# Performance work log

Hardware: AMD Instinct MI355X
Metric: run time of the kernel (lower is better)

## Reference

```python
import jax, jax.numpy as jnp
import numpy as np

W = 50          # Sakoe-Chiba window half-width (|i-j| <= W)
BIG = 1e9       # finite 'infinity' so gradients stay NaN-free
EPS = 1e-8      # matches torch.cosine_similarity eps


def setup_inputs() -> dict:
    key = jax.random.key(0)
    k1, k2 = jax.random.split(key)
    x1 = jax.random.normal(k1, (64, 512, 256), dtype=jnp.float32)
    x2 = jax.random.normal(k2, (64, 512, 256), dtype=jnp.float32)
    return {"x1": x1, "x2": x2}


def _cosine_cost(x1, x2):
    # cost[b,i,j] = 1 - cos_sim(x1[b,i], x2[b,j])
    num = jnp.einsum('bid,bjd->bij', x1, x2)
    n1 = jnp.maximum(jnp.sqrt(jnp.sum(x1 * x1, axis=-1)), EPS)  # [B,T1]
    n2 = jnp.maximum(jnp.sqrt(jnp.sum(x2 * x2, axis=-1)), EPS)  # [B,T2]
    return 1.0 - num / (n1[:, :, None] * n2[:, None, :])


def _dtw_acc(cost, w):
    # Anti-diagonal wavefront DP: acc[i,j] = cost[i,j] + min(acc[i-1,j], acc[i,j-1], acc[i-1,j-1])
    # with the Sakoe-Chiba band |i-j| <= w. Returns acc[T1-1, T2-1] per batch.
    B, T1, T2 = cost.shape
    ii = jnp.arange(T1)
    dt = cost.dtype

    def step(carry, d):
        prev1, prev2 = carry                       # diagonals d-1 and d-2, each [B,T1] indexed by i
        jj = d - ii                                # column index for each row i on diagonal d
        valid = (jj >= 0) & (jj < T2) & (jnp.abs(ii - jj) <= w)
        # gather cost[b, i, d-i]
        cdiag = jnp.take_along_axis(
            cost, jnp.clip(jj, 0, T2 - 1)[None, :, None], axis=2)[..., 0]  # [B,T1]
        pad = jnp.full((B, 1), BIG, dt)
        p1_im1 = jnp.concatenate([pad, prev1[:, :-1]], axis=1)  # acc[i-1, j]   (diag d-1, i-1)
        p2_im1 = jnp.concatenate([pad, prev2[:, :-1]], axis=1)  # acc[i-1, j-1] (diag d-2, i-1)
        m = jnp.minimum(jnp.minimum(prev1, p1_im1), p2_im1)     # prev1 = acc[i, j-1]
        m = jnp.where((ii == 0) & (jj == 0), jnp.zeros((), dt), m)  # DP origin
        new = jnp.where(valid, cdiag + m, jnp.full((), BIG, dt))
        return (new, prev1), None

    init = (jnp.full((B, T1), BIG, dt), jnp.full((B, T1), BIG, dt))
    (last, _), _ = jax.lax.scan(step, init, jnp.arange(T1 + T2 - 1))
    return last[:, T1 - 1]  # acc[-1, -1]


def reference(x1, x2):
    cost = _cosine_cost(x1, x2)       # [B,T1,T2]
    scores = _dtw_acc(cost, W)        # [B]
    return scores[:, None]            # [B,1], matches unsqueeze(-1)
```

## Files before the change

kernel.cpp:

```cpp
#include <hip/hip_runtime.h>

#define BIGF 1e9f
#define TT 512
#define DD 256
#define NB 64
#define DROWS 1088
#define SAK 40
#define CST 66

typedef float floatx16 __attribute__((ext_vector_type(16)));
typedef __bf16 bf16x8 __attribute__((ext_vector_type(8)));

__device__ __forceinline__ float dpp_wave_shr1(float x, float oldv) {
  int r = __builtin_amdgcn_update_dpp(__builtin_bit_cast(int, oldv),
                                      __builtin_bit_cast(int, x),
                                      0x138, 0xF, 0xF, false);
  return __builtin_bit_cast(float, r);
}
__device__ __forceinline__ float dpp_wave_shl1(float x, float oldv) {
  int r = __builtin_amdgcn_update_dpp(__builtin_bit_cast(int, oldv),
                                      __builtin_bit_cast(int, x),
                                      0x130, 0xF, 0xF, false);
  return __builtin_bit_cast(float, r);
}

__global__ __launch_bounds__(256) void cost_kernel(const float* __restrict__ x1,
                                                   const float* __restrict__ x2,
                                                   float* __restrict__ diag) {
  const int n = blockIdx.x;
  const int b = n & 63;
  const int m = n >> 6;
  const int it = m & 7;
  const int jt = m >> 3;
  const int i0 = it * 64;
  const int j0 = i0 - 50 + jt * 64;

  __shared__ __align__(16) float sC[64 * CST];
  __bf16* sA = (__bf16*)sC;
  __bf16* sB = ((__bf16*)sC) + 64 * SAK;
  __shared__ float rA[64];
  __shared__ float rB[64];

  const int t = threadIdx.x;
  const int lane = t & 63;
  const int w = t >> 6;
  const int wi = w >> 1;
  const int wj = w & 1;
  const int ln = lane & 31;
  const int kh = lane >> 5;

  float* db = diag + (size_t)b * (DROWS * 64);

  if (m == 0) {
    for (int r = w; r < 180; r += 4) {
      const int d = (r < 64) ? r : r + 908;
      const int p = d & 1;
      const int i = (d >> 1) + lane + p - 25;
      const int j = d - i;
      const int k = 2 * lane + p;
      if (k > 100 || (unsigned)i >= TT || (unsigned)j >= TT)
        db[(size_t)d * 64 + lane] = BIGF;
    }
  }

  const int sr = t >> 2;
  const int sq = t & 3;
  const float* x1b = x1 + (size_t)b * (TT * DD);
  const float* x2b = x2 + (size_t)b * (TT * DD);
  int gj = j0 + sr;
  gj = gj < 0 ? 0 : (gj > TT - 1 ? TT - 1 : gj);
  const float* pAg = x1b + (size_t)(i0 + sr) * DD + sq * 8;
  const float* pBg = x2b + (size_t)gj * DD + sq * 8;
  __bf16* dA = sA + sr * SAK + sq * 8;
  __bf16* dB = sB + sr * SAK + sq * 8;

  const __bf16* fAp = sA + (wi * 32 + ln) * SAK + kh * 8;
  const __bf16* fBp = sB + (wj * 32 + ln) * SAK + kh * 8;

  floatx16 acc = {};
  float pa = 0.f, pb = 0.f;

  for (int kc = 0; kc < DD; kc += 32) {
    const float4 a0 = *(const float4*)(pAg + kc);
    const float4 a1 = *(const float4*)(pAg + kc + 4);
    const float4 b0 = *(const float4*)(pBg + kc);
    const float4 b1 = *(const float4*)(pBg + kc + 4);
    pa += a0.x * a0.x + a0.y * a0.y + a0.z * a0.z + a0.w * a0.w;
    pa += a1.x * a1.x + a1.y * a1.y + a1.z * a1.z + a1.w * a1.w;
    pb += b0.x * b0.x + b0.y * b0.y + b0.z * b0.z + b0.w * b0.w;
    pb += b1.x * b1.x + b1.y * b1.y + b1.z * b1.z + b1.w * b1.w;
    __syncthreads();
    {
      bf16x8 va, vb;
      va[0] = (__bf16)a0.x; va[1] = (__bf16)a0.y; va[2] = (__bf16)a0.z; va[3] = (__bf16)a0.w;
      va[4] = (__bf16)a1.x; va[5] = (__bf16)a1.y; va[6] = (__bf16)a1.z; va[7] = (__bf16)a1.w;
      vb[0] = (__bf16)b0.x; vb[1] = (__bf16)b0.y; vb[2] = (__bf16)b0.z; vb[3] = (__bf16)b0.w;
      vb[4] = (__bf16)b1.x; vb[5] = (__bf16)b1.y; vb[6] = (__bf16)b1.z; vb[7] = (__bf16)b1.w;
      *(bf16x8*)dA = va;
      *(bf16x8*)dB = vb;
    }
    __syncthreads();
    const bf16x8 fa0 = *(const bf16x8*)fAp;
    const bf16x8 fb0 = *(const bf16x8*)fBp;
    const bf16x8 fa1 = *(const bf16x8*)(fAp + 16);
    const bf16x8 fb1 = *(const bf16x8*)(fBp + 16);
    acc = __builtin_amdgcn_mfma_f32_32x32x16_bf16(fa0, fb0, acc, 0, 0, 0);
    acc = __builtin_amdgcn_mfma_f32_32x32x16_bf16(fa1, fb1, acc, 0, 0, 0);
  }

  pa += __shfl_xor(pa, 1, 64); pa += __shfl_xor(pa, 2, 64);
  pb += __shfl_xor(pb, 1, 64); pb += __shfl_xor(pb, 2, 64);
  if (sq == 0) {
    rA[sr] = 1.0f / fmaxf(sqrtf(pa), 1e-8f);
    rB[sr] = 1.0f / fmaxf(sqrtf(pb), 1e-8f);
  }
  __syncthreads();

  {
    const int rj = wj * 32 + ln;
    const float r2 = rB[rj];
#pragma unroll
    for (int reg = 0; reg < 16; ++reg) {
      const int ri = wi * 32 + (reg & 3) + 8 * (reg >> 2) + 4 * kh;
      sC[ri * CST + rj] = 1.0f - acc[reg] * rA[ri] * r2;
    }
  }
  __syncthreads();

  {
    const int d0 = i0 + j0;
    const int a65 = 65 * lane;
#pragma unroll 4
    for (int rr = 0; rr < 32; ++rr) {
      const int r = 4 * rr + w;
      const int d = d0 + r;
      const int p = d & 1;
      const int roff = ((d + p - 50) >> 1) - i0;
      const int ri = lane + roff;
      const int rj = r - ri;
      const int kband = 2 * lane + p;
      const int jg = j0 + rj;
      if (((unsigned)ri < 64u) & ((unsigned)rj < 64u) & (kband <= 100) &
          ((unsigned)jg < (unsigned)TT)) {
        db[(size_t)d * 64 + lane] = sC[a65 + 65 * roff + r];
      }
    }
  }
}

__global__ __launch_bounds__(64) void dtw_dp_kernel(const float* __restrict__ diag,
                                                    float* __restrict__ out) {
  const int b = blockIdx.x;
  const int l = threadIdx.x;
  const bool inv_odd = (l >= 50);
  const bool inv_even = (l >= 51);
  const float* base = diag + (size_t)b * (DROWS * 64);
  const float* pO = base + 64 + l;
  const float* pE = base + 128 + l;
  float cr[32];
#pragma unroll
  for (int t = 0; t < 16; ++t) {
    cr[2 * t] = *pO; pO += 128;
    cr[2 * t + 1] = *pE; pE += 128;
  }
  float prev2 = BIGF;
  const float c00 = base[25];
  float prev1 = (l == 25) ? c00 : BIGF;
  float ans = BIGF;
  for (int it = 0; it < 32; ++it) {
#pragma unroll
    for (int u = 0; u < 16; ++u) {
      const float c1 = inv_odd ? BIGF : cr[2 * u];
      cr[2 * u] = *pO; pO += 128;
      const float sh = dpp_wave_shl1(prev1, BIGF);
      const float m3 = fminf(fminf(prev1, sh), prev2);
      prev2 = prev1;
      prev1 = c1 + m3;
      const float c2 = inv_even ? BIGF : cr[2 * u + 1];
      cr[2 * u + 1] = *pE; pE += 128;
      const float sh2 = dpp_wave_shr1(prev1, BIGF);
      const float m32 = fminf(fminf(sh2, prev1), prev2);
      prev2 = prev1;
      prev1 = c2 + m32;
      if (u == 14 && it == 31) ans = prev1;
    }
  }
  if (l == 25) out[b] = ans;
}

extern "C" void kernel_launch(void* const* d_in, const int* in_sizes, int n_in,
                              void* d_out, int out_size, void* d_ws, size_t ws_size,
                              hipStream_t stream) {
  const float* x1 = (const float*)d_in[0];
  const float* x2 = (const float*)d_in[1];
  float* out = (float*)d_out;
  float* diag = (float*)d_ws;

  cost_kernel<<<NB * 24, 256, 0, stream>>>(x1, x2, diag);
  dtw_dp_kernel<<<NB, 64, 0, stream>>>(diag, out);
}
```

Baseline: 127.1 us.

## Process two cost tiles per block and deepen DP cost prefetch

The cost kernel now launches 768 blocks, each handling two 64x64 tiles in a loop. Tiles are remapped so consecutive blocks cover 8 different batches. This cuts the launch to roughly 3 blocks per CU and changes how loads spread across memory. The DP kernel doubles its register prefetch buffer from 32 to 64 cost values to hide more global load latency, at the cost of more registers and a deeper prologue.

```diff
diff --git a/kernel.cpp b/kernel.cpp
--- a/kernel.cpp
+++ b/kernel.cpp
@@ -27,13 +27,9 @@
 __global__ __launch_bounds__(256) void cost_kernel(const float* __restrict__ x1,
                                                    const float* __restrict__ x2,
                                                    float* __restrict__ diag) {
-  const int n = blockIdx.x;
-  const int b = n & 63;
-  const int m = n >> 6;
-  const int it = m & 7;
-  const int jt = m >> 3;
-  const int i0 = it * 64;
-  const int j0 = i0 - 50 + jt * 64;
+  const int p = blockIdx.x;
+  const int x = p & 7;
+  const int pl = p >> 3;
 
   __shared__ __align__(16) float sC[64 * CST];
   __bf16* sA = (__bf16*)sC;
@@ -49,100 +45,111 @@
   const int ln = lane & 31;
   const int kh = lane >> 5;
 
-  float* db = diag + (size_t)b * (DROWS * 64);
-
-  if (m == 0) {
-    for (int r = w; r < 180; r += 4) {
-      const int d = (r < 64) ? r : r + 908;
-      const int p = d & 1;
-      const int i = (d >> 1) + lane + p - 25;
-      const int j = d - i;
-      const int k = 2 * lane + p;
-      if (k > 100 || (unsigned)i >= TT || (unsigned)j >= TT)
-        db[(size_t)d * 64 + lane] = BIGF;
-    }
-  }
-
   const int sr = t >> 2;
   const int sq = t & 3;
-  const float* x1b = x1 + (size_t)b * (TT * DD);
-  const float* x2b = x2 + (size_t)b * (TT * DD);
-  int gj = j0 + sr;
-  gj = gj < 0 ? 0 : (gj > TT - 1 ? TT - 1 : gj);
-  const float* pAg = x1b + (size_t)(i0 + sr) * DD + sq * 8;
-  const float* pBg = x2b + (size_t)gj * DD + sq * 8;
   __bf16* dA = sA + sr * SAK + sq * 8;
   __bf16* dB = sB + sr * SAK + sq * 8;
-
   const __bf16* fAp = sA + (wi * 32 + ln) * SAK + kh * 8;
   const __bf16* fBp = sB + (wj * 32 + ln) * SAK + kh * 8;
 
-  floatx16 acc = {};
-  float pa = 0.f, pb = 0.f;
-
-  for (int kc = 0; kc < DD; kc += 32) {
-    const float4 a0 = *(const float4*)(pAg + kc);
-    const float4 a1 = *(const float4*)(pAg + kc + 4);
-    const float4 b0 = *(const float4*)(pBg + kc);
-    const float4 b1 = *(const float4*)(pBg + kc + 4);
-    pa += a0.x * a0.x + a0.y * a0.y + a0.z * a0.z + a0.w * a0.w;
-    pa += a1.x * a1.x + a1.y * a1.y + a1.z * a1.z + a1.w * a1.w;
-    pb += b0.x * b0.x + b0.y * b0.y + b0.z * b0.z + b0.w * b0.w;
-    pb += b1.x * b1.x + b1.y * b1.y + b1.z * b1.z + b1.w * b1.w;
+  for (int kt = 0; kt < 2; ++kt) {
+    const int T = pl + 96 * kt;
+    const int bhi = T / 24;
+    const int m = T - bhi * 24;
+    const int b = bhi * 8 + x;
+    const int it = m & 7;
+    const int jt = m >> 3;
+    const int i0 = it * 64;
+    const int j0 = i0 - 50 + jt * 64;
+
+    float* db = diag + (size_t)b * (DROWS * 64);
+
+    if (m == 0) {
+      for (int r = w; r < 180; r += 4) {
+        const int d = (r < 64) ? r : r + 908;
+        const int pp = d & 1;
+        const int i = (d >> 1) + lane + pp - 25;
+        const int j = d - i;
+        const int k = 2 * lane + pp;
+        if (k > 100 || (unsigned)i >= TT || (unsigned)j >= TT)
+          db[(size_t)d * 64 + lane] = BIGF;
+      }
+    }
+
+    const float* x1b = x1 + (size_t)b * (TT * DD);
+    const float* x2b = x2 + (size_t)b * (TT * DD);
+    int gj = j0 + sr;
+    gj = gj < 0 ? 0 : (gj > TT - 1 ? TT - 1 : gj);
+    const float* pAg = x1b + (size_t)(i0 + sr) * DD + sq * 8;
+    const float* pBg = x2b + (size_t)gj * DD + sq * 8;
+
+    floatx16 acc = {};
+    float pa = 0.f, pb = 0.f;
+
+    for (int kc = 0; kc < DD; kc += 32) {
+      const float4 a0 = *(const float4*)(pAg + kc);
+      const float4 a1 = *(const float4*)(pAg + kc + 4);
+      const float4 b0 = *(const float4*)(pBg + kc);
+      const float4 b1 = *(const float4*)(pBg + kc + 4);
+      pa += a0.x * a0.x + a0.y * a0.y + a0.z * a0.z + a0.w * a0.w;
+      pa += a1.x * a1.x + a1.y * a1.y + a1.z * a1.z + a1.w * a1.w;
+      pb += b0.x * b0.x + b0.y * b0.y + b0.z * b0.z + b0.w * b0.w;
+      pb += b1.x * b1.x + b1.y * b1.y + b1.z * b1.z + b1.w * b1.w;
+      __syncthreads();
+      {
+        bf16x8 va, vb;
+        va[0] = (__bf16)a0.x; va[1] = (__bf16)a0.y; va[2] = (__bf16)a0.z; va[3] = (__bf16)a0.w;
+        va[4] = (__bf16)a1.x; va[5] = (__bf16)a1.y; va[6] = (__bf16)a1.z; va[7] = (__bf16)a1.w;
+        vb[0] = (__bf16)b0.x; vb[1] = (__bf16)b0.y; vb[2] = (__bf16)b0.z; vb[3] = (__bf16)b0.w;
+        vb[4] = (__bf16)b1.x; vb[5] = (__bf16)b1.y; vb[6] = (__bf16)b1.z; vb[7] = (__bf16)b1.w;
+        *(bf16x8*)dA = va;
+        *(bf16x8*)dB = vb;
+      }
+      __syncthreads();
+      const bf16x8 fa0 = *(const bf16x8*)fAp;
+      const bf16x8 fb0 = *(const bf16x8*)fBp;
+      const bf16x8 fa1 = *(const bf16x8*)(fAp + 16);
+      const bf16x8 fb1 = *(const bf16x8*)(fBp + 16);
+      acc = __builtin_amdgcn_mfma_f32_32x32x16_bf16(fa0, fb0, acc, 0, 0, 0);
+      acc = __builtin_amdgcn_mfma_f32_32x32x16_bf16(fa1, fb1, acc, 0, 0, 0);
+    }
+
+    pa += __shfl_xor(pa, 1, 64); pa += __shfl_xor(pa, 2, 64);
+    pb += __shfl_xor(pb, 1, 64); pb += __shfl_xor(pb, 2, 64);
+    if (sq == 0) {
+      rA[sr] = 1.0f / fmaxf(sqrtf(pa), 1e-8f);
+      rB[sr] = 1.0f / fmaxf(sqrtf(pb), 1e-8f);
+    }
     __syncthreads();
+
     {
-      bf16x8 va, vb;
-      va[0] = (__bf16)a0.x; va[1] = (__bf16)a0.y; va[2] = (__bf16)a0.z; va[3] = (__bf16)a0.w;
-      va[4] = (__bf16)a1.x; va[5] = (__bf16)a1.y; va[6] = (__bf16)a1.z; va[7] = (__bf16)a1.w;
-      vb[0] = (__bf16)b0.x; vb[1] = (__bf16)b0.y; vb[2] = (__bf16)b0.z; vb[3] = (__bf16)b0.w;
-      vb[4] = (__bf16)b1.x; vb[5] = (__bf16)b1.y; vb[6] = (__bf16)b1.z; vb[7] = (__bf16)b1.w;
-      *(bf16x8*)dA = va;
-      *(bf16x8*)dB = vb;
+      const int rj = wj * 32 + ln;
+      const float r2 = rB[rj];
+#pragma unroll
+      for (int reg = 0; reg < 16; ++reg) {
+        const int ri = wi * 32 + (reg & 3) + 8 * (reg >> 2) + 4 * kh;
+        sC[ri * CST + rj] = 1.0f - acc[reg] * rA[ri] * r2;
+      }
     }
     __syncthreads();
-    const bf16x8 fa0 = *(const bf16x8*)fAp;
-    const bf16x8 fb0 = *(const bf16x8*)fBp;
-    const bf16x8 fa1 = *(const bf16x8*)(fAp + 16);
-    const bf16x8 fb1 = *(const bf16x8*)(fBp + 16);
-    acc = __builtin_amdgcn_mfma_f32_32x32x16_bf16(fa0, fb0, acc, 0, 0, 0);
-    acc = __builtin_amdgcn_mfma_f32_32x32x16_bf16(fa1, fb1, acc, 0, 0, 0);
-  }
-
-  pa += __shfl_xor(pa, 1, 64); pa += __shfl_xor(pa, 2, 64);
-  pb += __shfl_xor(pb, 1, 64); pb += __shfl_xor(pb, 2, 64);
-  if (sq == 0) {
-    rA[sr] = 1.0f / fmaxf(sqrtf(pa), 1e-8f);
-    rB[sr] = 1.0f / fmaxf(sqrtf(pb), 1e-8f);
-  }
-  __syncthreads();
-
-  {
-    const int rj = wj * 32 + ln;
-    const float r2 = rB[rj];
-#pragma unroll
-    for (int reg = 0; reg < 16; ++reg) {
-      const int ri = wi * 32 + (reg & 3) + 8 * (reg >> 2) + 4 * kh;
-      sC[ri * CST + rj] = 1.0f - acc[reg] * rA[ri] * r2;
-    }
-  }
-  __syncthreads();
-
-  {
-    const int d0 = i0 + j0;
-    const int a65 = 65 * lane;
+
+    {
+      const int d0 = i0 + j0;
+      const int a65 = 65 * lane;
 #pragma unroll 4
-    for (int rr = 0; rr < 32; ++rr) {
-      const int r = 4 * rr + w;
-      const int d = d0 + r;
-      const int p = d & 1;
-      const int roff = ((d + p - 50) >> 1) - i0;
-      const int ri = lane + roff;
-      const int rj = r - ri;
-      const int kband = 2 * lane + p;
-      const int jg = j0 + rj;
-      if (((unsigned)ri < 64u) & ((unsigned)rj < 64u) & (kband <= 100) &
-          ((unsigned)jg < (unsigned)TT)) {
-        db[(size_t)d * 64 + lane] = sC[a65 + 65 * roff + r];
+      for (int rr = 0; rr < 32; ++rr) {
+        const int r = 4 * rr + w;
+        const int d = d0 + r;
+        const int pp = d & 1;
+        const int roff = ((d + pp - 50) >> 1) - i0;
+        const int ri = lane + roff;
+        const int rj = r - ri;
+        const int kband = 2 * lane + pp;
+        const int jg = j0 + rj;
+        if (((unsigned)ri < 64u) & ((unsigned)rj < 64u) & (kband <= 100) &
+            ((unsigned)jg < (unsigned)TT)) {
+          db[(size_t)d * 64 + lane] = sC[a65 + 65 * roff + r];
+        }
       }
     }
   }
@@ -157,9 +164,9 @@
   const float* base = diag + (size_t)b * (DROWS * 64);
   const float* pO = base + 64 + l;
   const float* pE = base + 128 + l;
-  float cr[32];
+  float cr[64];
 #pragma unroll
-  for (int t = 0; t < 16; ++t) {
+  for (int t = 0; t < 32; ++t) {
     cr[2 * t] = *pO; pO += 128;
     cr[2 * t + 1] = *pE; pE += 128;
   }
@@ -167,9 +174,9 @@
   const float c00 = base[25];
   float prev1 = (l == 25) ? c00 : BIGF;
   float ans = BIGF;
-  for (int it = 0; it < 32; ++it) {
+  for (int itr = 0; itr < 16; ++itr) {
 #pragma unroll
-    for (int u = 0; u < 16; ++u) {
+    for (int u = 0; u < 32; ++u) {
       const float c1 = inv_odd ? BIGF : cr[2 * u];
       cr[2 * u] = *pO; pO += 128;
       const float sh = dpp_wave_shl1(prev1, BIGF);
@@ -182,7 +189,7 @@
       const float m32 = fminf(fminf(sh2, prev1), prev2);
       prev2 = prev1;
       prev1 = c2 + m32;
-      if (u == 14 && it == 31) ans = prev1;
+      if (itr == 15 && u == 30) ans = prev1;
     }
   }
   if (l == 25) out[b] = ans;
@@ -196,6 +203,6 @@
   float* out = (float*)d_out;
   float* diag = (float*)d_ws;
 
-  cost_kernel<<<NB * 24, 256, 0, stream>>>(x1, x2, diag);
+  cost_kernel<<<768, 256, 0, stream>>>(x1, x2, diag);
   dtw_dp_kernel<<<NB, 64, 0, stream>>>(diag, out);
 }
```

Result: no change. 126.6 us (-0.4%).
